# Optimization experiments

Hardware: AMD Instinct MI355X
Metric: run time of the kernel (lower is better)

The kernel has to match this reference:

```python
import jax, jax.numpy as jnp
import numpy as np

# CycleFC1w1a constants (from init_kwargs / gen_offset)
IN_CH = 384
KH, KW = 1, 7  # cycle kernel; actual conv weight is 1x1
START = (KH * KW) // 2  # 3


def _gen_offset_x(C):
    # kernel_size[0] == 1 branch: off_y = 0, off_x[i] = (i + START) % KW - KW // 2
    i = jnp.arange(C)
    return (i + START) % KW - KW // 2  # int32, values in [-3, 3]


def setup_inputs() -> dict:
    key = jax.random.key(0)
    k1, k2, k3 = jax.random.split(key, 3)
    x = jax.random.normal(k1, (64, IN_CH, 32, 32), dtype=jnp.float32)
    weight = jax.random.normal(k2, (IN_CH, IN_CH), dtype=jnp.float32) * 0.05  # [out_ch, in_ch]
    bias = jax.random.normal(k3, (IN_CH,), dtype=jnp.float32) * 0.01
    return {"x": x, "weight": weight, "bias": bias}


def reference(x, weight, bias):
    B, C, H, W = x.shape
    # BinaryQuantizer forward: sign()
    xb = jnp.sign(x)
    wb = jnp.sign(weight)  # [O, C]

    # Fixed per-channel integer horizontal offsets -> exact shifted gather
    off_x = _gen_offset_x(C)                                  # [C]
    cols = jnp.arange(W)[None, :] + off_x[:, None]            # [C, W] sample col = w + off
    valid = (cols >= 0) & (cols < W)                          # zero-pad out of bounds
    cols_c = jnp.clip(cols, 0, W - 1)
    # gather along width per channel: [B, C, H, W]
    g = jnp.take_along_axis(xb, cols_c[None, :, None, :], axis=3)
    g = g * valid[None, :, None, :].astype(x.dtype)

    # pointwise (1x1) channel-mixing conv
    out = jnp.einsum('bchw,oc->bohw', g, wb) + bias[None, :, None, None]
    return out
```

## Files before the change

### kernel.cpp

```cpp
#include <hip/hip_runtime.h>
#include <stdint.h>


#define IN_CH 384
#define HH 32
#define WW 32
#define BB 64
#define HR 2

constexpr uint64_t P7(int t) {
  uint64_t m = 0;
  for (int k = 0; k < 64; ++k)
    if (k % 7 == t) m |= (1ull << k);
  return m;
}
__device__ __constant__ uint64_t Pm[7] = {P7(0), P7(1), P7(2), P7(3), P7(4), P7(5), P7(6)};

__global__ __launch_bounds__(64) void cyc_prep(const float* __restrict__ wgt,
                                               const float* __restrict__ bias,
                                               uint64_t* __restrict__ wbg,
                                               float* __restrict__ bias2) {
  const int o = blockIdx.x;
  const int lane = threadIdx.x;
  __shared__ uint64_t wb_sh[6];
#pragma unroll
  for (int j = 0; j < 6; ++j) {
    uint64_t m = __ballot(wgt[o * IN_CH + j * 64 + lane] < 0.0f);
    if (lane == 0) wb_sh[j] = m;
  }
  __syncthreads();
  if (lane < 6) wbg[o * 6 + lane] = wb_sh[lane];
  if (lane < WW) {
    const int w = lane;
    int nv = 0, corr = 0;
#pragma unroll
    for (int j = 0; j < 6; ++j) {
      uint64_t V = 0;
#pragma unroll
      for (int d = -3; d <= 3; ++d) {
        int wd = w + d;
        if (wd >= 0 && wd < WW) V |= Pm[(d - j + 14) % 7];
      }
      nv += __popcll(V);
      corr += __popcll(wb_sh[j] & ~V);
    }
    bias2[o * WW + w] = bias[o] + (float)nv + 2.0f * (float)corr;
  }
}

__global__ __launch_bounds__(768) void cyc_main(const float* __restrict__ x,
                                                const uint64_t* __restrict__ wbg,
                                                const float* __restrict__ bias2,
                                                float* __restrict__ out) {
  __shared__ uint64_t sh_X[HR][WW][6];
  __shared__ uint64_t sh_G[HR][WW][6];
  const int t = threadIdx.x;
  const int b = blockIdx.x >> 4;
  const int h0 = (blockIdx.x & 15) * HR;
  const int wave = t >> 6, lane = t & 63;

  {
    const int j = wave % 6, r = wave / 6;
    const int c = j * 64 + lane;
    const float4* xp = reinterpret_cast<const float4*>(
        x + (size_t)((b * IN_CH + c) * HH + h0 + r) * WW);
    unsigned myw = 0;
#pragma unroll
    for (int i = 0; i < 8; ++i) {
      float4 v = xp[i];
      myw |= (v.x < 0.0f ? 1u : 0u) << (i * 4 + 0);
      myw |= (v.y < 0.0f ? 1u : 0u) << (i * 4 + 1);
      myw |= (v.z < 0.0f ? 1u : 0u) << (i * 4 + 2);
      myw |= (v.w < 0.0f ? 1u : 0u) << (i * 4 + 3);
    }
#pragma unroll
    for (int w = 0; w < WW; ++w) {
      uint64_t m = __ballot((myw >> w) & 1u);
      if (lane == 0) sh_X[r][w][j] = m;
    }
  }
  __syncthreads();

  if (t < HR * WW * 6) {
    const int r = t / (WW * 6);
    const int q = t % (WW * 6);
    const int w = q & 31, j = q >> 5;
    uint64_t g = 0;
#pragma unroll
    for (int d = -3; d <= 3; ++d) {
      int wd = w + d;
      if (wd >= 0 && wd < WW) g |= sh_X[r][wd][j] & Pm[(d - j + 14) % 7];
    }
    sh_G[r][w][j] = g;
  }
  __syncthreads();

  const int og = __builtin_amdgcn_readfirstlane(wave);
  const int w = lane & 31, r = lane >> 5;
  uint64_t g0, g1, g2, g3, g4, g5;
  {
    const ulonglong2* gv = reinterpret_cast<const ulonglong2*>(&sh_G[r][w][0]);
    ulonglong2 a = gv[0], bq = gv[1], cq = gv[2];
    g0 = a.x; g1 = a.y; g2 = bq.x; g3 = bq.y; g4 = cq.x; g5 = cq.y;
  }
  float* op = out + ((size_t)b * IN_CH + og * 32) * (HH * WW) + h0 * WW + lane;
  const uint64_t* wp = wbg + og * 32 * 6;
  const float* bp = bias2 + og * 32 * WW + w;
#pragma unroll 4
  for (int i = 0; i < 32; ++i) {
    const uint64_t w0 = wp[i * 6 + 0], w1 = wp[i * 6 + 1], w2 = wp[i * 6 + 2];
    const uint64_t w3 = wp[i * 6 + 3], w4 = wp[i * 6 + 4], w5 = wp[i * 6 + 5];
    int mm = __popcll(g0 ^ w0) + __popcll(g1 ^ w1) + __popcll(g2 ^ w2) +
             __popcll(g3 ^ w3) + __popcll(g4 ^ w4) + __popcll(g5 ^ w5);
    op[i * (HH * WW)] = bp[i * WW] - 2.0f * (float)mm;
  }
}

extern "C" void kernel_launch(void* const* d_in, const int* in_sizes, int n_in,
                              void* d_out, int out_size, void* d_ws, size_t ws_size,
                              hipStream_t stream) {
  const float* x = (const float*)d_in[0];
  const float* wgt = (const float*)d_in[1];
  const float* bias = (const float*)d_in[2];
  float* out = (float*)d_out;

  uint64_t* wbg = (uint64_t*)d_ws;
  float* bias2 = (float*)((char*)d_ws + IN_CH * 6 * sizeof(uint64_t));

  cyc_prep<<<IN_CH, 64, 0, stream>>>(wgt, bias, wbg, bias2);
  cyc_main<<<BB * (HH / HR), 768, 0, stream>>>(x, wbg, bias2, out);
}
```

Measured before the change: 200.1 us.

## Process four rows per block and preload transposed bias into registers

Each block now covers four image rows instead of two, halving the grid. Every thread computes two output rows per weight load, so each weight word fetched is reused twice. The per-column bias is stored transposed so each thread loads its 32 bias values as contiguous float4 vectors into registers, instead of strided loads inside the loop. The cost is higher register pressure (two sets of activation words, a 32-float bias array, full unroll) and fewer blocks to spread across the GPU.

```diff
diff --git a/kernel.cpp b/kernel.cpp
--- a/kernel.cpp
+++ b/kernel.cpp
@@ -6,7 +6,7 @@
 #define HH 32
 #define WW 32
 #define BB 64
-#define HR 2
+#define HR 4
 
 constexpr uint64_t P7(int t) {
   uint64_t m = 0;
@@ -19,7 +19,7 @@
 __global__ __launch_bounds__(64) void cyc_prep(const float* __restrict__ wgt,
                                                const float* __restrict__ bias,
                                                uint64_t* __restrict__ wbg,
-                                               float* __restrict__ bias2) {
+                                               float* __restrict__ bias2t) {
   const int o = blockIdx.x;
   const int lane = threadIdx.x;
   __shared__ uint64_t wb_sh[6];
@@ -44,23 +44,25 @@
       nv += __popcll(V);
       corr += __popcll(wb_sh[j] & ~V);
     }
-    bias2[o * WW + w] = bias[o] + (float)nv + 2.0f * (float)corr;
+    bias2t[w * IN_CH + o] = bias[o] + (float)nv + 2.0f * (float)corr;
   }
 }
 
 __global__ __launch_bounds__(768) void cyc_main(const float* __restrict__ x,
                                                 const uint64_t* __restrict__ wbg,
-                                                const float* __restrict__ bias2,
+                                                const float* __restrict__ bias2t,
                                                 float* __restrict__ out) {
   __shared__ uint64_t sh_X[HR][WW][6];
   __shared__ uint64_t sh_G[HR][WW][6];
   const int t = threadIdx.x;
-  const int b = blockIdx.x >> 4;
-  const int h0 = (blockIdx.x & 15) * HR;
+  const int b = blockIdx.x >> 3;
+  const int h0 = (blockIdx.x & 7) * HR;
   const int wave = t >> 6, lane = t & 63;
 
-  {
-    const int j = wave % 6, r = wave / 6;
+#pragma unroll
+  for (int p = 0; p < 2; ++p) {
+    const int tau = wave + p * 12;
+    const int r = tau / 6, j = tau % 6;
     const int c = j * 64 + lane;
     const float4* xp = reinterpret_cast<const float4*>(
         x + (size_t)((b * IN_CH + c) * HH + h0 + r) * WW);
@@ -81,7 +83,7 @@
   }
   __syncthreads();
 
-  if (t < HR * WW * 6) {
+  {
     const int r = t / (WW * 6);
     const int q = t % (WW * 6);
     const int w = q & 31, j = q >> 5;
@@ -96,23 +98,37 @@
   __syncthreads();
 
   const int og = __builtin_amdgcn_readfirstlane(wave);
-  const int w = lane & 31, r = lane >> 5;
-  uint64_t g0, g1, g2, g3, g4, g5;
+  const int w = lane & 31, r2 = lane >> 5;
+  uint64_t gA[6], gB[6];
   {
-    const ulonglong2* gv = reinterpret_cast<const ulonglong2*>(&sh_G[r][w][0]);
-    ulonglong2 a = gv[0], bq = gv[1], cq = gv[2];
-    g0 = a.x; g1 = a.y; g2 = bq.x; g3 = bq.y; g4 = cq.x; g5 = cq.y;
+    const ulonglong2* gv = reinterpret_cast<const ulonglong2*>(&sh_G[r2][w][0]);
+    ulonglong2 a0 = gv[0], a1 = gv[1], a2 = gv[2];
+    gA[0] = a0.x; gA[1] = a0.y; gA[2] = a1.x; gA[3] = a1.y; gA[4] = a2.x; gA[5] = a2.y;
+    const ulonglong2* hv = reinterpret_cast<const ulonglong2*>(&sh_G[2 + r2][w][0]);
+    ulonglong2 b0 = hv[0], b1 = hv[1], b2 = hv[2];
+    gB[0] = b0.x; gB[1] = b0.y; gB[2] = b1.x; gB[3] = b1.y; gB[4] = b2.x; gB[5] = b2.y;
   }
-  float* op = out + ((size_t)b * IN_CH + og * 32) * (HH * WW) + h0 * WW + lane;
+  float bb[32];
+  {
+    const float4* bsrc =
+        reinterpret_cast<const float4*>(bias2t + w * IN_CH + og * 32);
+    float4* bdst = reinterpret_cast<float4*>(bb);
+#pragma unroll
+    for (int i = 0; i < 8; ++i) bdst[i] = bsrc[i];
+  }
+  float* opA = out + ((size_t)b * IN_CH + og * 32) * (HH * WW) + h0 * WW + lane;
+  float* opB = opA + 2 * WW;
   const uint64_t* wp = wbg + og * 32 * 6;
-  const float* bp = bias2 + og * 32 * WW + w;
-#pragma unroll 4
+#pragma unroll
   for (int i = 0; i < 32; ++i) {
     const uint64_t w0 = wp[i * 6 + 0], w1 = wp[i * 6 + 1], w2 = wp[i * 6 + 2];
     const uint64_t w3 = wp[i * 6 + 3], w4 = wp[i * 6 + 4], w5 = wp[i * 6 + 5];
-    int mm = __popcll(g0 ^ w0) + __popcll(g1 ^ w1) + __popcll(g2 ^ w2) +
-             __popcll(g3 ^ w3) + __popcll(g4 ^ w4) + __popcll(g5 ^ w5);
-    op[i * (HH * WW)] = bp[i * WW] - 2.0f * (float)mm;
+    int mmA = __popcll(gA[0] ^ w0) + __popcll(gA[1] ^ w1) + __popcll(gA[2] ^ w2) +
+              __popcll(gA[3] ^ w3) + __popcll(gA[4] ^ w4) + __popcll(gA[5] ^ w5);
+    int mmB = __popcll(gB[0] ^ w0) + __popcll(gB[1] ^ w1) + __popcll(gB[2] ^ w2) +
+              __popcll(gB[3] ^ w3) + __popcll(gB[4] ^ w4) + __popcll(gB[5] ^ w5);
+    opA[i * (HH * WW)] = bb[i] - 2.0f * (float)mmA;
+    opB[i * (HH * WW)] = bb[i] - 2.0f * (float)mmB;
   }
 }
 
@@ -125,8 +141,8 @@
   float* out = (float*)d_out;
 
   uint64_t* wbg = (uint64_t*)d_ws;
-  float* bias2 = (float*)((char*)d_ws + IN_CH * 6 * sizeof(uint64_t));
+  float* bias2t = (float*)((char*)d_ws + IN_CH * 6 * sizeof(uint64_t));
 
-  cyc_prep<<<IN_CH, 64, 0, stream>>>(wgt, bias, wbg, bias2);
-  cyc_main<<<BB * (HH / HR), 768, 0, stream>>>(x, wbg, bias2, out);
+  cyc_prep<<<IN_CH, 64, 0, stream>>>(wgt, bias, wbg, bias2t);
+  cyc_main<<<BB * (HH / HR), 768, 0, stream>>>(x, wbg, bias2t, out);
 }
```

Result: faster. 195.6 us (-2.3%).
